# Performance work log

Measured on AMD Instinct MI355X. Metric: run time of the kernel, lower is better.

## Reference

```python
import jax, jax.numpy as jnp
import numpy as np

EPS = 1e-08

def setup_inputs() -> dict:
    key = jax.random.key(0)
    k1, k2 = jax.random.split(key)
    h = jax.random.normal(k1, (4096, 512), dtype=jnp.float32)   # [B, D]
    A = jax.random.normal(k2, (32768, 512), dtype=jnp.float32)  # [K, D]
    return {"h": h, "A": A}

def _l2_normalize(x, eps=EPS):
    # matches torch F.normalize(p=2): x / max(||x||, eps)
    n = jnp.sqrt(jnp.sum(x * x, axis=-1, keepdims=True))
    return x / jnp.maximum(n, eps)

def reference(h, A):
    # cosine metric: normalize both, matmul, argmax over K
    h_n = _l2_normalize(h)                      # [B, D]
    A_n = _l2_normalize(A)                      # [K, D]
    scores = jnp.einsum('bd,kd->bk', h_n, A_n)  # [B, K]
    idx = jnp.argmax(scores, axis=1, keepdims=True)  # [B, 1] int
    return idx
```

## Files before the change

kernel.cpp:

```cpp
#include <hip/hip_runtime.h>
#include <stdint.h>


#define DIM 512
#define B_ROWS 4096
#define K_ROWS 32768
#define BT 128
#define KT 128
#define NKT (K_ROWS / KT)
#define KSLOTS 32
#define NCHUNK 4
#define QSCALE (127.0f / 0.26f)

typedef __attribute__((ext_vector_type(4))) float fx4;
typedef __attribute__((ext_vector_type(4))) int int4v;
typedef unsigned long long u64;

__device__ __forceinline__ uint32_t ford(float s) {
    uint32_t u = __float_as_uint(s);
    return u ^ ((uint32_t)((int32_t)u >> 31) | 0x80000000u);
}
__device__ __forceinline__ u64 umax64(u64 a, u64 b) { return a > b ? a : b; }
__device__ __forceinline__ u64 umin64(u64 a, u64 b) { return a < b ? a : b; }
__device__ __forceinline__ uint32_t umax32(uint32_t a, uint32_t b) { return a > b ? a : b; }
__device__ __forceinline__ uint32_t umin32(uint32_t a, uint32_t b) { return a < b ? a : b; }

__device__ __forceinline__ int q8(float x, float qs) {
    int v = __float2int_rn(x * qs);
    return v < -127 ? -127 : (v > 127 ? 127 : v);
}

__global__ __launch_bounds__(256) void prep_kernel(const float* __restrict__ A,
                                                   const float* __restrict__ h,
                                                   char* __restrict__ a8,
                                                   char* __restrict__ h8,
                                                   float* __restrict__ rn) {
    const int lane = threadIdx.x & 63, wid = threadIdx.x >> 6;
    const bool isA = blockIdx.x < 8192;
    const int row = (isA ? blockIdx.x : blockIdx.x - 8192) * 4 + wid;
    const float* src = (isA ? A : h) + (size_t)row * DIM;
    char* dst = (isA ? a8 : h8) + (size_t)row * DIM;

    const fx4* p = (const fx4*)src;
    fx4 a = p[lane * 2], b = p[lane * 2 + 1];
    float ss = a[0]*a[0] + a[1]*a[1] + a[2]*a[2] + a[3]*a[3]
             + b[0]*b[0] + b[1]*b[1] + b[2]*b[2] + b[3]*b[3];
    #pragma unroll
    for (int off = 32; off > 0; off >>= 1) ss += __shfl_xor(ss, off, 64);
    float r = 1.0f / fmaxf(sqrtf(ss), 1e-8f);
    if (isA && lane == 0) rn[row] = r;

    float qs = r * QSCALE;
    int v0 = q8(a[0], qs), v1 = q8(a[1], qs), v2 = q8(a[2], qs), v3 = q8(a[3], qs);
    int v4 = q8(b[0], qs), v5 = q8(b[1], qs), v6 = q8(b[2], qs), v7 = q8(b[3], qs);
    uint32_t lo = (uint32_t)(v0 & 255) | ((uint32_t)(v1 & 255) << 8)
                | ((uint32_t)(v2 & 255) << 16) | ((uint32_t)(v3 & 255) << 24);
    uint32_t hi = (uint32_t)(v4 & 255) | ((uint32_t)(v5 & 255) << 8)
                | ((uint32_t)(v6 & 255) << 16) | ((uint32_t)(v7 & 255) << 24);
    *reinterpret_cast<uint2*>(dst + lane * 8) = make_uint2(lo, hi);
}

typedef __attribute__((address_space(3))) uint32_t lds_u32;
typedef __attribute__((address_space(1))) const uint32_t g_u32;

__global__ __launch_bounds__(256, 2) void score_kernel(
    const char* __restrict__ h8, const char* __restrict__ a8,
    u64* __restrict__ cand)
{
    __shared__ __attribute__((aligned(16))) char smem[65536];

    const int t = threadIdx.x, lane = t & 63, wid = t >> 6;
    const int wm = wid >> 1, wn = wid & 1;
    const int lr = lane & 15, q = lane >> 4;
    const int btile = blockIdx.x >> 5, kslot = blockIdx.x & 31;
    const int b0 = btile * BT;

    const int srow = lane >> 3;
    const int scol = (lane & 7) ^ srow;
    const int s7 = lr & 7;
    const int sw0 = (q ^ s7) * 16;
    const int sw1 = ((4 + q) ^ s7) * 16;

    const char* hsrc = h8 + (size_t)b0 * DIM;

    uint32_t v1[16], v2[16];
    #pragma unroll
    for (int s = 0; s < 16; s++) { v1[s] = 0u; v2[s] = 0u; }

    auto stage = [&](int cc, int buf) {
        const int kt = kslot + (cc >> 2) * KSLOTS;
        const int dcc = cc & 3;
        const char* asrc = a8 + (size_t)(kt * KT) * DIM;
        char* hb = smem + buf * 32768;
        char* ab = hb + 16384;
        #pragma unroll
        for (int i = 0; i < 4; i++) {
            int issue = wid * 4 + i;
            size_t roff = (size_t)(issue * 8 + srow) * DIM + dcc * 128 + scol * 16;
            __builtin_amdgcn_global_load_lds((g_u32*)(hsrc + roff),
                (lds_u32*)(hb + issue * 1024), 16, 0, 0);
            __builtin_amdgcn_global_load_lds((g_u32*)(asrc + roff),
                (lds_u32*)(ab + issue * 1024), 16, 0, 0);
        }
    };

    stage(0, 0);
    __syncthreads();

    #pragma unroll 1
    for (int it = 0; it < 8; it++) {
        int4v acc[4][4];
        #pragma unroll
        for (int mi = 0; mi < 4; mi++)
            #pragma unroll
            for (int ni = 0; ni < 4; ni++)
                acc[mi][ni] = (int4v){0, 0, 0, 0};

        #pragma unroll
        for (int dc = 0; dc < 4; dc++) {
            const int c = it * 4 + dc;
            if (dc < 3 || it < 7) stage(c + 1, (dc & 1) ^ 1);

            const char* hf = smem + (dc & 1) * 32768;
            const char* af = hf + 16384;

            int4v af0[4], af1[4];
            #pragma unroll
            for (int ni = 0; ni < 4; ni++) {
                const char* base = af + (wn * 64 + ni * 16 + lr) * 128;
                af0[ni] = *reinterpret_cast<const int4v*>(base + sw0);
                af1[ni] = *reinterpret_cast<const int4v*>(base + sw1);
            }
            #pragma unroll
            for (int mi = 0; mi < 4; mi++) {
                const char* base = hf + (wm * 64 + mi * 16 + lr) * 128;
                int4v h0 = *reinterpret_cast<const int4v*>(base + sw0);
                int4v h1 = *reinterpret_cast<const int4v*>(base + sw1);
                #pragma unroll
                for (int ni = 0; ni < 4; ni++) {
                    acc[mi][ni] = __builtin_amdgcn_mfma_i32_16x16x64_i8(h0, af0[ni], acc[mi][ni], 0, 0, 0);
                    acc[mi][ni] = __builtin_amdgcn_mfma_i32_16x16x64_i8(h1, af1[ni], acc[mi][ni], 0, 0, 0);
                }
            }

            if (dc == 3) {
                const uint32_t metabase = (uint32_t)(it << 2);
                #pragma unroll
                for (int mi = 0; mi < 4; mi++)
                    #pragma unroll
                    for (int ni = 0; ni < 4; ni++) {
                        const uint32_t meta = metabase | (uint32_t)ni;
                        #pragma unroll
                        for (int r = 0; r < 4; r++) {
                            uint32_t ord = (uint32_t)acc[mi][ni][r] ^ 0x80000000u;
                            uint32_t pk = (ord & 0xFFFFFFC0u) | meta;
                            int s = mi * 4 + r;
                            uint32_t lo = umin32(v1[s], pk);
                            v1[s] = umax32(v1[s], pk);
                            v2[s] = umax32(v2[s], lo);
                        }
                    }
            }

            __syncthreads();
        }
    }

    uint32_t* cl = (uint32_t*)smem;
    u64 g1 = 0, g2 = 0, g3 = 0;
    for (int pass = 0; pass < 2; pass++) {
        __syncthreads();
        #pragma unroll
        for (int s = 0; s < 16; s++) {
            int mi = s >> 2, r = s & 3;
            int row_local = wm * 64 + mi * 16 + q * 4 + r;
            cl[row_local * 33 + wn * 16 + lr] = pass ? v2[s] : v1[s];
        }
        __syncthreads();
        if (t < BT) {
            #pragma unroll 4
            for (int j = 0; j < 32; j++) {
                uint32_t pv = cl[t * 33 + j];
                uint32_t meta = pv & 63u;
                int k = (kslot + (int)(meta >> 2) * KSLOTS) * KT
                      + (j >> 4) * 64 + (int)(meta & 3u) * 16 + (j & 15);
                u64 e = ((u64)(pv & 0xFFFFFFC0u) << 32) | (u64)(~(uint32_t)k);
                u64 t1 = umax64(g1, e), t2 = umin64(g1, e);
                g3 = umax64(g3, umin64(g2, t2));
                g2 = umax64(g2, t2);
                g1 = t1;
            }
        }
    }
    if (t < BT) {
        size_t base = ((size_t)(b0 + t) * KSLOTS + kslot) * 3;
        cand[base] = g1;
        cand[base + 1] = g2;
        cand[base + 2] = g3;
    }
}

__global__ __launch_bounds__(256) void refine_kernel(
    const float* __restrict__ h, const float* __restrict__ A,
    const float* __restrict__ rn, const u64* __restrict__ cand,
    int* __restrict__ out)
{
    const int t = threadIdx.x, lane = t & 63, wid = t >> 6;
    const int row = blockIdx.x * 4 + wid;
    const u64* cr = cand + (size_t)row * (KSLOTS * 3);
    u64 x0 = cr[lane];
    u64 x1 = (lane < KSLOTS * 3 - 64) ? cr[64 + lane] : 0ULL;

    u64 sel[8];
    #pragma unroll
    for (int j = 0; j < 8; j++) {
        u64 v = umax64(x0, x1);
        #pragma unroll
        for (int m = 32; m >= 1; m >>= 1) v = umax64(v, __shfl_xor(v, m, 64));
        sel[j] = v;
        if (x0 == v) x0 = 0;
        else if (x1 == v) x1 = 0;
    }

    const fx4* hp = reinterpret_cast<const fx4*>(h + (size_t)row * DIM);
    fx4 h0 = hp[lane * 2], h1 = hp[lane * 2 + 1];

    u64 best = 0;
    #pragma unroll
    for (int j = 0; j < 8; j++) {
        uint32_t kg = ~(uint32_t)sel[j];
        const fx4* ap = reinterpret_cast<const fx4*>(A + (size_t)kg * DIM);
        fx4 a0 = ap[lane * 2], a1 = ap[lane * 2 + 1];
        float s = h0[0]*a0[0] + h0[1]*a0[1] + h0[2]*a0[2] + h0[3]*a0[3]
                + h1[0]*a1[0] + h1[1]*a1[1] + h1[2]*a1[2] + h1[3]*a1[3];
        #pragma unroll
        for (int m = 32; m >= 1; m >>= 1) s += __shfl_xor(s, m, 64);
        s *= rn[kg];
        u64 pk = ((u64)ford(s) << 32) | (u64)(~kg);
        best = umax64(best, pk);
    }
    if (lane == 0) out[row] = (int)(~(uint32_t)best);
}

extern "C" void kernel_launch(void* const* d_in, const int* in_sizes, int n_in,
                              void* d_out, int out_size, void* d_ws, size_t ws_size,
                              hipStream_t stream) {
    const float* h = (const float*)d_in[0];
    const float* A = (const float*)d_in[1];
    int* out = (int*)d_out;

    char* w = (char*)d_ws;
    char* a8 = w;
    char* h8 = w + (size_t)K_ROWS * DIM;
    float* rn = (float*)(w + (size_t)(K_ROWS + B_ROWS) * DIM);
    u64* cand = (u64*)(w + (size_t)(K_ROWS + B_ROWS) * DIM
                         + (size_t)K_ROWS * sizeof(float));

    prep_kernel<<<8192 + 1024, 256, 0, stream>>>(A, h, a8, h8, rn);
    score_kernel<<<32 * KSLOTS, 256, 0, stream>>>(h8, a8, cand);
    refine_kernel<<<B_ROWS / 4, 256, 0, stream>>>(h, A, rn, cand, out);
}
```

Baseline: 198.7 us.

## Keep h tile resident in registers and stream only A through LDS

Each block's 128-row h tile is the same across all iterations, so each wave now loads its 64 rows of quantized h (full 512 D) once into registers (32 int4 vectors) instead of re-staging h through shared memory every chunk. LDS drops from 64KB to 32KB and only A tiles are double-buffered. The MFMA loop is also split into two half-K passes, so fewer A fragments are live at once. This removes repeated h global and LDS traffic but adds 128 VGPRs per thread, which risks spills or lower occupancy under the 256x2 launch bounds.

```diff
diff --git a/kernel.cpp b/kernel.cpp
--- a/kernel.cpp
+++ b/kernel.cpp
@@ -67,7 +67,7 @@
     const char* __restrict__ h8, const char* __restrict__ a8,
     u64* __restrict__ cand)
 {
-    __shared__ __attribute__((aligned(16))) char smem[65536];
+    __shared__ __attribute__((aligned(16))) char smem[32768];
 
     const int t = threadIdx.x, lane = t & 63, wid = t >> 6;
     const int wm = wid >> 1, wn = wid & 1;
@@ -81,30 +81,39 @@
     const int sw0 = (q ^ s7) * 16;
     const int sw1 = ((4 + q) ^ s7) * 16;
 
-    const char* hsrc = h8 + (size_t)b0 * DIM;
-
     uint32_t v1[16], v2[16];
     #pragma unroll
     for (int s = 0; s < 16; s++) { v1[s] = 0u; v2[s] = 0u; }
 
-    auto stage = [&](int cc, int buf) {
+    auto stageA = [&](int cc, int buf) {
         const int kt = kslot + (cc >> 2) * KSLOTS;
         const int dcc = cc & 3;
         const char* asrc = a8 + (size_t)(kt * KT) * DIM;
-        char* hb = smem + buf * 32768;
-        char* ab = hb + 16384;
+        char* ab = smem + buf * 16384;
         #pragma unroll
         for (int i = 0; i < 4; i++) {
             int issue = wid * 4 + i;
             size_t roff = (size_t)(issue * 8 + srow) * DIM + dcc * 128 + scol * 16;
-            __builtin_amdgcn_global_load_lds((g_u32*)(hsrc + roff),
-                (lds_u32*)(hb + issue * 1024), 16, 0, 0);
             __builtin_amdgcn_global_load_lds((g_u32*)(asrc + roff),
                 (lds_u32*)(ab + issue * 1024), 16, 0, 0);
         }
     };
 
-    stage(0, 0);
+    stageA(0, 0);
+
+    int4v hreg[4][2][4];
+    {
+        const char* hbase = h8 + (size_t)(b0 + wm * 64 + lr) * DIM + q * 16;
+        #pragma unroll
+        for (int dc = 0; dc < 4; dc++)
+            #pragma unroll
+            for (int kh = 0; kh < 2; kh++)
+                #pragma unroll
+                for (int mi = 0; mi < 4; mi++)
+                    hreg[dc][kh][mi] = *reinterpret_cast<const int4v*>(
+                        hbase + (size_t)mi * 16 * DIM + dc * 128 + kh * 64);
+    }
+
     __syncthreads();
 
     #pragma unroll 1
@@ -119,29 +128,33 @@
         #pragma unroll
         for (int dc = 0; dc < 4; dc++) {
             const int c = it * 4 + dc;
-            if (dc < 3 || it < 7) stage(c + 1, (dc & 1) ^ 1);
-
-            const char* hf = smem + (dc & 1) * 32768;
-            const char* af = hf + 16384;
-
-            int4v af0[4], af1[4];
-            #pragma unroll
-            for (int ni = 0; ni < 4; ni++) {
-                const char* base = af + (wn * 64 + ni * 16 + lr) * 128;
-                af0[ni] = *reinterpret_cast<const int4v*>(base + sw0);
-                af1[ni] = *reinterpret_cast<const int4v*>(base + sw1);
-            }
-            #pragma unroll
-            for (int mi = 0; mi < 4; mi++) {
-                const char* base = hf + (wm * 64 + mi * 16 + lr) * 128;
-                int4v h0 = *reinterpret_cast<const int4v*>(base + sw0);
-                int4v h1 = *reinterpret_cast<const int4v*>(base + sw1);
-                #pragma unroll
-                for (int ni = 0; ni < 4; ni++) {
-                    acc[mi][ni] = __builtin_amdgcn_mfma_i32_16x16x64_i8(h0, af0[ni], acc[mi][ni], 0, 0, 0);
-                    acc[mi][ni] = __builtin_amdgcn_mfma_i32_16x16x64_i8(h1, af1[ni], acc[mi][ni], 0, 0, 0);
-                }
-            }
+            if (dc < 3 || it < 7) stageA(c + 1, (dc & 1) ^ 1);
+
+            const char* af = smem + (dc & 1) * 16384;
+
+            int4v af0[4];
+            #pragma unroll
+            for (int ni = 0; ni < 4; ni++)
+                af0[ni] = *reinterpret_cast<const int4v*>(
+                    af + (wn * 64 + ni * 16 + lr) * 128 + sw0);
+            #pragma unroll
+            for (int mi = 0; mi < 4; mi++)
+                #pragma unroll
+                for (int ni = 0; ni < 4; ni++)
+                    acc[mi][ni] = __builtin_amdgcn_mfma_i32_16x16x64_i8(
+                        hreg[dc][0][mi], af0[ni], acc[mi][ni], 0, 0, 0);
+
+            int4v af1[4];
+            #pragma unroll
+            for (int ni = 0; ni < 4; ni++)
+                af1[ni] = *reinterpret_cast<const int4v*>(
+                    af + (wn * 64 + ni * 16 + lr) * 128 + sw1);
+            #pragma unroll
+            for (int mi = 0; mi < 4; mi++)
+                #pragma unroll
+                for (int ni = 0; ni < 4; ni++)
+                    acc[mi][ni] = __builtin_amdgcn_mfma_i32_16x16x64_i8(
+                        hreg[dc][1][mi], af1[ni], acc[mi][ni], 0, 0, 0);
 
             if (dc == 3) {
                 const uint32_t metabase = (uint32_t)(it << 2);
```

New measurement: 232.7 us. 1.17x slower.
